# Kernel tuning notes

Measured on AMD Instinct MI355X. Metric: run time of the kernel, lower is better.

Reference implementation:

```python
import jax, jax.numpy as jnp
import numpy as np

N = 100000      # nodes
E = 3_200_000   # edges
F_IN = 256      # input feature dim
R = 16          # rank_bound (GCN output dim)
D = 128         # embedding_dim (trans output)
B = 16384       # batch of node indices
EPS = 1e-5


def setup_inputs() -> dict:
    key = jax.random.key(0)
    ks = jax.random.split(key, 9)
    x = jax.random.normal(ks[0], (N, F_IN), jnp.float32)
    edge_index = jax.random.randint(ks[1], (2, E), 0, N, dtype=jnp.int64)
    trans = jax.random.normal(ks[2], (R, D), jnp.float32) * 0.1
    batch = jax.random.randint(ks[3], (B,), 0, N, dtype=jnp.int64)
    W = jax.random.normal(ks[4], (R, F_IN), jnp.float32) / np.sqrt(F_IN).astype(np.float32)
    b = jnp.zeros((R,), jnp.float32)
    ln_w = jnp.ones((R,), jnp.float32)
    ln_b = jnp.zeros((R,), jnp.float32)
    prelu_a = jnp.full((1,), 0.25, jnp.float32)  # PReLU single shared slope
    return dict(x=x, edge_index=edge_index, trans=trans, batch=batch,
                W=W, b=b, ln_w=ln_w, ln_b=ln_b, prelu_a=prelu_a)


def gcn_conv(x, edge_index, W, b):
    # PyG GCNConv: lin first, then symmetric-normalized aggregation with self-loops.
    h = x @ W.T  # [N, R]
    loop = jnp.arange(N, dtype=edge_index.dtype)
    src = jnp.concatenate([edge_index[0], loop])  # messages flow src -> dst
    dst = jnp.concatenate([edge_index[1], loop])
    deg = jax.ops.segment_sum(jnp.ones_like(dst, h.dtype), dst, num_segments=N)
    dinv = jnp.where(deg > 0, jax.lax.rsqrt(deg), 0.0)
    norm = dinv[src] * dinv[dst]                   # [E+N]
    msg = h[src] * norm[:, None]                   # gather [E+N, R]
    out = jax.ops.segment_sum(msg, dst, num_segments=N)  # scatter-add
    return out + b


def reference(x, edge_index, trans, batch, W, b, ln_w, ln_b, prelu_a):
    h = gcn_conv(x, edge_index, W, b)              # [N, R]
    # PyG LayerNorm (graph mode): normalize over all nodes and channels.
    h = h - h.mean()
    var = (h * h).mean()
    h = h * jax.lax.rsqrt(var + EPS) * ln_w + ln_b
    # PReLU
    h = jnp.where(h >= 0, h, prelu_a * h)
    emb = h @ trans                                # [N, D]
    return emb[batch]                              # index_select(0, batch)
```

## Files before the change

### kernel.cpp

```cpp
#include <hip/hip_runtime.h>

#define EPS 1e-5f
#define BSHIFT 8
#define BSIZE  256
#define NBMAX  512
#define PCHUNK 8192
#define LCAP   12288

__device__ __forceinline__ unsigned short f2bf(float f) {
    unsigned u = __float_as_uint(f);
    u += 0x7FFFu + ((u >> 16) & 1u);
    return (unsigned short)(u >> 16);
}
__device__ __forceinline__ float bf2f(unsigned short s) {
    return __uint_as_float(((unsigned)s) << 16);
}
__device__ __forceinline__ void acc8(float* acc, uint4 v) {
    acc[0] += bf2f((unsigned short)(v.x & 0xFFFFu)); acc[1] += bf2f((unsigned short)(v.x >> 16));
    acc[2] += bf2f((unsigned short)(v.y & 0xFFFFu)); acc[3] += bf2f((unsigned short)(v.y >> 16));
    acc[4] += bf2f((unsigned short)(v.z & 0xFFFFu)); acc[5] += bf2f((unsigned short)(v.z >> 16));
    acc[6] += bf2f((unsigned short)(v.w & 0xFFFFu)); acc[7] += bf2f((unsigned short)(v.w >> 16));
}

__global__ __launch_bounds__(512) void k_zero(unsigned* ghist, int NB) {
    int t = threadIdx.x;
    if (t < NB) ghist[t] = 0u;
}

__global__ __launch_bounds__(512) void k_bhist(const int* __restrict__ ei,
                                               unsigned* __restrict__ ghist,
                                               unsigned* __restrict__ blkhist,
                                               int E, int NB) {
    __shared__ unsigned sh[NBMAX];
    int t = threadIdx.x;
    for (int i = t; i < NB; i += 512) sh[i] = 0u;
    __syncthreads();
    const int4* dst4 = (const int4*)(ei + E);
    int E4 = E >> 2;
    int base4 = blockIdx.x * (PCHUNK / 4);
#pragma unroll
    for (int i = 0; i < PCHUNK / 4 / 512; i++) {
        int idx = base4 + i * 512 + t;
        if (idx < E4) {
            int4 d = dst4[idx];
            atomicAdd(&sh[d.x >> BSHIFT], 1u);
            atomicAdd(&sh[d.y >> BSHIFT], 1u);
            atomicAdd(&sh[d.z >> BSHIFT], 1u);
            atomicAdd(&sh[d.w >> BSHIFT], 1u);
        }
    }
    __syncthreads();
    unsigned* bh = blkhist + (size_t)blockIdx.x * NBMAX;
    for (int i = t; i < NB; i += 512) {
        unsigned c = sh[i];
        bh[i] = c;
        if (c) atomicAdd(&ghist[i], c);
    }
}

__global__ __launch_bounds__(512) void k_bscan(const unsigned* __restrict__ ghist,
                                               unsigned* __restrict__ base,
                                               unsigned* __restrict__ cursor,
                                               unsigned* __restrict__ nstart,
                                               int NB, int N, int E) {
    __shared__ unsigned sh[512];
    int t = threadIdx.x;
    unsigned v = (t < NB) ? ghist[t] : 0u;
    sh[t] = v;
    __syncthreads();
    for (int off = 1; off < 512; off <<= 1) {
        unsigned a = (t >= off) ? sh[t - off] : 0u;
        __syncthreads();
        sh[t] += a;
        __syncthreads();
    }
    if (t < NB) { unsigned ex = sh[t] - v; base[t] = ex; cursor[t] = ex; }
    if (t == 0) { base[NB] = (unsigned)E; nstart[N] = (unsigned)E; }
}

__global__ __launch_bounds__(512) void k_bpart(const int* __restrict__ ei,
                                               const unsigned* __restrict__ blkhist,
                                               unsigned* __restrict__ cursor,
                                               unsigned* __restrict__ sorted, int E, int NB) {
    __shared__ unsigned cnt[NBMAX];
    __shared__ unsigned lbase[NBMAX];
    __shared__ unsigned loff[NBMAX + 1];
    __shared__ unsigned sh[512];
    __shared__ unsigned stage[PCHUNK];
    __shared__ unsigned short bkt[PCHUNK];
    int t = threadIdx.x;
    const unsigned* bh = blkhist + (size_t)blockIdx.x * NBMAX;
    for (int i = t; i < NB; i += 512) cnt[i] = bh[i];
    __syncthreads();
    const int4* src4 = (const int4*)ei;
    const int4* dst4 = (const int4*)(ei + E);
    int E4 = E >> 2;
    int base4 = blockIdx.x * (PCHUNK / 4);
    unsigned v = (t < NB) ? cnt[t] : 0u;
    sh[t] = v;
    if (t < NB) lbase[t] = v ? atomicAdd(&cursor[t], v) : 0u;
    __syncthreads();
    for (int off = 1; off < 512; off <<= 1) {
        unsigned a = (t >= off) ? sh[t - off] : 0u;
        __syncthreads();
        sh[t] += a;
        __syncthreads();
    }
    if (t < NB) { loff[t] = sh[t] - v; cnt[t] = 0u; }
    if (t == NB - 1) loff[NB] = sh[t];
    __syncthreads();
    for (int b = t; b < NB; b += 512) {
        unsigned s = loff[b], e2 = loff[b + 1];
        for (unsigned j = s; j < e2; j++) bkt[j] = (unsigned short)b;
    }
#pragma unroll
    for (int i = 0; i < PCHUNK / 4 / 512; i++) {
        int idx = base4 + i * 512 + t;
        if (idx < E4) {
            int4 s = src4[idx];
            int4 d = dst4[idx];
            int b; unsigned r;
            b = d.x >> BSHIFT; r = atomicAdd(&cnt[b], 1u);
            stage[loff[b] + r] = (unsigned)s.x | ((unsigned)(d.x & (BSIZE - 1)) << 17);
            b = d.y >> BSHIFT; r = atomicAdd(&cnt[b], 1u);
            stage[loff[b] + r] = (unsigned)s.y | ((unsigned)(d.y & (BSIZE - 1)) << 17);
            b = d.z >> BSHIFT; r = atomicAdd(&cnt[b], 1u);
            stage[loff[b] + r] = (unsigned)s.z | ((unsigned)(d.z & (BSIZE - 1)) << 17);
            b = d.w >> BSHIFT; r = atomicAdd(&cnt[b], 1u);
            stage[loff[b] + r] = (unsigned)s.w | ((unsigned)(d.w & (BSIZE - 1)) << 17);
        }
    }
    __syncthreads();
    unsigned total = loff[NB];
    for (unsigned i = t; i < total; i += 512) {
        unsigned b = bkt[i];
        sorted[lbase[b] + (i - loff[b])] = stage[i];
    }
}

__global__ __launch_bounds__(256) void k_bdeg2(const unsigned* __restrict__ base,
                                               const unsigned* __restrict__ sorted,
                                               unsigned* __restrict__ nstart,
                                               float* __restrict__ dinv, int N) {
    __shared__ unsigned deg[BSIZE];
    int b = blockIdx.x, t = threadIdx.x;
    deg[t] = 0u;
    __syncthreads();
    unsigned s0 = base[b], s1 = base[b + 1];
    for (unsigned j = s0 + t; j < s1; j += 256)
        atomicAdd(&deg[sorted[j] >> 17], 1u);
    __syncthreads();
    unsigned d0 = deg[t];
    int lane = t & 63, wid = t >> 6;
    unsigned inc = d0;
    for (int off = 1; off < 64; off <<= 1) {
        unsigned u = __shfl_up(inc, off, 64);
        if (lane >= off) inc += u;
    }
    __shared__ unsigned wsum[4];
    if (lane == 63) wsum[wid] = inc;
    __syncthreads();
    unsigned wbase = 0;
    for (int w = 0; w < wid; w++) wbase += wsum[w];
    unsigned excl = wbase + inc - d0;
    int node = (b << BSHIFT) + t;
    if (node < N) {
        nstart[node] = s0 + excl;
        dinv[node] = rsqrtf((float)(d0 + 1u));
    }
}

__global__ __launch_bounds__(256) void k_gemm(const float* __restrict__ x,
                                              const float* __restrict__ W,
                                              const float* __restrict__ dinv,
                                              unsigned short* __restrict__ hs, int N) {
    __shared__ float ws[16 * 256];
    int t = threadIdx.x;
    for (int i = t; i < 1024; i += 256) ((float4*)ws)[i] = ((const float4*)W)[i];
    __syncthreads();
    int node = blockIdx.x * 256 + t;
    if (node >= N) return;
    const float4* xr = (const float4*)(x + (size_t)node * 256);
    float acc[16];
#pragma unroll
    for (int r = 0; r < 16; r++) acc[r] = 0.f;
#pragma unroll 4
    for (int k = 0; k < 64; k++) {
        float4 a = xr[k];
#pragma unroll
        for (int r = 0; r < 16; r++) {
            float4 w = ((const float4*)ws)[r * 64 + k];
            acc[r] += a.x * w.x + a.y * w.y + a.z * w.z + a.w * w.w;
        }
    }
    float dv = dinv[node];
    unsigned pk[8];
#pragma unroll
    for (int i = 0; i < 8; i++)
        pk[i] = (unsigned)f2bf(acc[2 * i] * dv) | ((unsigned)f2bf(acc[2 * i + 1] * dv) << 16);
    uint4* dst = (uint4*)(hs + (size_t)node * 16);
    dst[0] = make_uint4(pk[0], pk[1], pk[2], pk[3]);
    dst[1] = make_uint4(pk[4], pk[5], pk[6], pk[7]);
}

__global__ __launch_bounds__(256) void k_aggf(const unsigned* __restrict__ base,
                                              const unsigned* __restrict__ nstart,
                                              const unsigned* __restrict__ sorted,
                                              const unsigned short* __restrict__ hs,
                                              const float* __restrict__ dinv,
                                              const float* __restrict__ bias,
                                              float* __restrict__ agg,
                                              float2* __restrict__ part,
                                              unsigned* __restrict__ scratch, int N) {
    __shared__ unsigned buf[LCAP];
    __shared__ unsigned cur0[BSIZE + 1];
    __shared__ unsigned curv[BSIZE];
    __shared__ float ss[4], qq[4];
    int b = blockIdx.x, t = threadIdx.x;
    unsigned s0 = base[b], s1 = base[b + 1];
    unsigned len = s1 - s0;
    int node = (b << BSHIFT) + t;
    unsigned ns = (node < N) ? nstart[node] : s1;
    cur0[t] = ns - s0;
    curv[t] = ns - s0;
    if (t == 0) cur0[BSIZE] = len;
    __syncthreads();
    bool fit = (len <= (unsigned)LCAP);
    if (fit) {
        for (unsigned j = t; j < len; j += 256) {
            unsigned u = sorted[s0 + j];
            unsigned pos = atomicAdd(&curv[u >> 17], 1u);
            buf[pos] = u & 0x1FFFFu;
        }
    } else {
        for (unsigned j = t; j < len; j += 256) {
            unsigned u = sorted[s0 + j];
            unsigned pos = atomicAdd(&curv[u >> 17], 1u);
            scratch[s0 + pos] = u & 0x1FFFFu;
        }
    }
    __syncthreads();
    int g = t >> 4, r = t & 15;
    int sub = r >> 1;
    int half = r & 1;
    float sacc = 0.f, qacc = 0.f;
#pragma unroll 1
    for (int p = 0; p < 16; p++) {
        int dloc = p * 16 + g;
        int d = (b << BSHIFT) + dloc;
        float acc[8];
#pragma unroll
        for (int c = 0; c < 8; c++) acc[c] = 0.f;
        if (d < N) {
            unsigned l0 = cur0[dloc], l1 = cur0[dloc + 1];
            for (unsigned j = l0; j < l1; j += 16) {
                unsigned row0 = j + sub, row1 = j + 8 + sub;
                bool p0 = row0 < l1, p1 = row1 < l1;
                unsigned i0 = 0, i1 = 0;
                if (fit) {
                    if (p0) i0 = buf[row0];
                    if (p1) i1 = buf[row1];
                } else {
                    if (p0) i0 = scratch[s0 + row0];
                    if (p1) i1 = scratch[s0 + row1];
                }
                uint4 v0, v1;
                if (p0) v0 = ((const uint4*)(hs + (size_t)i0 * 16))[half];
                if (p1) v1 = ((const uint4*)(hs + (size_t)i1 * 16))[half];
                if (p0) acc8(acc, v0);
                if (p1) acc8(acc, v1);
            }
        }
#pragma unroll
        for (int off = 2; off <= 8; off <<= 1) {
#pragma unroll
            for (int c = 0; c < 8; c++) acc[c] += __shfl_down(acc[c], off, 64);
        }
        if (d < N && r < 2) {
            float dd = dinv[d];
            uint4 hv = ((const uint4*)(hs + (size_t)d * 16))[half];
            float self[8];
            self[0] = bf2f((unsigned short)(hv.x & 0xFFFFu)); self[1] = bf2f((unsigned short)(hv.x >> 16));
            self[2] = bf2f((unsigned short)(hv.y & 0xFFFFu)); self[3] = bf2f((unsigned short)(hv.y >> 16));
            self[4] = bf2f((unsigned short)(hv.z & 0xFFFFu)); self[5] = bf2f((unsigned short)(hv.z >> 16));
            self[6] = bf2f((unsigned short)(hv.w & 0xFFFFu)); self[7] = bf2f((unsigned short)(hv.w >> 16));
            float o[8];
#pragma unroll
            for (int c = 0; c < 8; c++) o[c] = (acc[c] + self[c]) * dd;
            float* an = agg + (size_t)d * 16 + half * 8;
            *(float4*)(an)     = make_float4(o[0], o[1], o[2], o[3]);
            *(float4*)(an + 4) = make_float4(o[4], o[5], o[6], o[7]);
            const float* bp = bias + half * 8;
            float4 b0 = *(const float4*)bp, b1 = *(const float4*)(bp + 4);
            float a0 = o[0] + b0.x, a1 = o[1] + b0.y, a2 = o[2] + b0.z, a3 = o[3] + b0.w;
            float a4 = o[4] + b1.x, a5 = o[5] + b1.y, a6 = o[6] + b1.z, a7 = o[7] + b1.w;
            sacc += (a0 + a1) + (a2 + a3) + (a4 + a5) + (a6 + a7);
            qacc += a0 * a0 + a1 * a1 + a2 * a2 + a3 * a3 + a4 * a4 + a5 * a5 + a6 * a6 + a7 * a7;
        }
    }
    for (int off = 32; off > 0; off >>= 1) {
        sacc += __shfl_down(sacc, off, 64);
        qacc += __shfl_down(qacc, off, 64);
    }
    int lane = t & 63, wid = t >> 6;
    if (lane == 0) { ss[wid] = sacc; qq[wid] = qacc; }
    __syncthreads();
    if (t == 0)
        part[b] = make_float2(ss[0] + ss[1] + ss[2] + ss[3],
                              qq[0] + qq[1] + qq[2] + qq[3]);
}

__global__ __launch_bounds__(256) void k_statsred(const float2* __restrict__ part,
                                                  float* __restrict__ scal, int M) {
    int t = threadIdx.x;
    float s = 0.f, q = 0.f;
    for (int i = t; i < M; i += 256) {
        float2 v = part[i];
        s += v.x; q += v.y;
    }
    for (int off = 32; off > 0; off >>= 1) {
        s += __shfl_down(s, off, 64);
        q += __shfl_down(q, off, 64);
    }
    __shared__ float ss[4], qq[4];
    int lane = t & 63, wid = t >> 6;
    if (lane == 0) { ss[wid] = s; qq[wid] = q; }
    __syncthreads();
    if (t == 0) {
        scal[0] = ss[0] + ss[1] + ss[2] + ss[3];
        scal[1] = qq[0] + qq[1] + qq[2] + qq[3];
    }
}

__global__ __launch_bounds__(256) void k_final(const float* __restrict__ agg,
                                               const int* __restrict__ batch,
                                               const float* __restrict__ trans,
                                               const float* __restrict__ bias,
                                               const float* __restrict__ ln_w,
                                               const float* __restrict__ ln_b,
                                               const float* __restrict__ prelu_a,
                                               const float* __restrict__ scal,
                                               float* __restrict__ out, int B, float invCnt) {
    __shared__ float tl[16 * 128];
    __shared__ float hh[8 * 16];
    const int tid = threadIdx.x;
    for (int i = tid; i < 2048; i += 256) tl[i] = trans[i];
    float mean = scal[0] * invCnt;
    float var  = scal[1] * invCnt - mean * mean;
    float inv  = rsqrtf(var + EPS);
    int row0 = blockIdx.x * 8;
    if (tid < 128) {
        int lr = tid >> 4, r = tid & 15;
        int row = row0 + lr;
        if (row < B) {
            int node = batch[row];
            float v = agg[(size_t)node * 16 + r] + bias[r];
            v = (v - mean) * inv * ln_w[r] + ln_b[r];
            float a = prelu_a[0];
            v = v >= 0.f ? v : a * v;
            hh[lr * 16 + r] = v;
        }
    }
    __syncthreads();
    int d = tid & 127, hlf = tid >> 7;
    float tv[16];
#pragma unroll
    for (int r = 0; r < 16; r++) tv[r] = tl[r * 128 + d];
#pragma unroll
    for (int rr = 0; rr < 4; rr++) {
        int lr = rr * 2 + hlf;
        int row = row0 + lr;
        if (row < B) {
            const float* hrow = hh + lr * 16;
            float acc = 0.f;
#pragma unroll
            for (int r = 0; r < 16; r++) acc += hrow[r] * tv[r];
            out[(size_t)row * 128 + d] = acc;
        }
    }
}

extern "C" void kernel_launch(void* const* d_in, const int* in_sizes, int n_in,
                              void* d_out, int out_size, void* d_ws, size_t ws_size,
                              hipStream_t stream) {
    const float* x       = (const float*)d_in[0];
    const int*   ei      = (const int*)d_in[1];
    const float* trans   = (const float*)d_in[2];
    const int*   batch   = (const int*)d_in[3];
    const float* W       = (const float*)d_in[4];
    const float* bias    = (const float*)d_in[5];
    const float* ln_w    = (const float*)d_in[6];
    const float* ln_b    = (const float*)d_in[7];
    const float* prelu_a = (const float*)d_in[8];
    float* out = (float*)d_out;

    const int N = in_sizes[0] / 256;
    const int E = in_sizes[1] / 2;
    const int B = in_sizes[3];
    const int NB = (N + BSIZE - 1) >> BSHIFT;
    const int pbp = (E + PCHUNK - 1) / PCHUNK;

    char* p = (char*)d_ws;
    unsigned short* hs = (unsigned short*)p;  p += (size_t)N * 16 * 2;
    float*    agg     = (float*)p;     p += (size_t)N * 16 * 4;
    unsigned* sorted  = (unsigned*)p;  p += (size_t)E * 4;
    unsigned* scratch = (unsigned*)p;  p += (size_t)E * 4;
    unsigned* blkhist = (unsigned*)p;  p += (size_t)pbp * NBMAX * 4;
    float*    dinv    = (float*)p;     p += (size_t)N * 4;
    unsigned* nstart  = (unsigned*)p;  p += (size_t)(N + 1) * 4;
    unsigned* ghist   = (unsigned*)p;  p += NBMAX * 4;
    unsigned* base    = (unsigned*)p;  p += (NBMAX + 1) * 4;
    unsigned* cursor  = (unsigned*)p;  p += NBMAX * 4;
    float*    scal    = (float*)p;     p += 2 * 4;
    p = (char*)(((size_t)p + 7) & ~(size_t)7);
    float2*   part    = (float2*)p;    p += (size_t)NB * 8;

    hipLaunchKernelGGL(k_zero,     dim3(1),               dim3(512), 0, stream, ghist, NB);
    hipLaunchKernelGGL(k_bhist,    dim3(pbp),             dim3(512), 0, stream, ei, ghist, blkhist, E, NB);
    hipLaunchKernelGGL(k_bscan,    dim3(1),               dim3(512), 0, stream, ghist, base, cursor, nstart, NB, N, E);
    hipLaunchKernelGGL(k_bpart,    dim3(pbp),             dim3(512), 0, stream, ei, blkhist, cursor, sorted, E, NB);
    hipLaunchKernelGGL(k_bdeg2,    dim3(NB),              dim3(256), 0, stream, base, sorted, nstart, dinv, N);
    hipLaunchKernelGGL(k_gemm,     dim3((N + 255) / 256), dim3(256), 0, stream, x, W, dinv, hs, N);
    hipLaunchKernelGGL(k_aggf,     dim3(NB),              dim3(256), 0, stream, base, nstart, sorted, hs, dinv, bias, agg, part, scratch, N);
    hipLaunchKernelGGL(k_statsred, dim3(1),               dim3(256), 0, stream, part, scal, NB);
    hipLaunchKernelGGL(k_final,    dim3((B + 7) / 8),     dim3(256), 0, stream, agg, batch, trans, bias,
                       ln_w, ln_b, prelu_a, scal, out, B, 1.0f / (float)(N * 16));
}
```

Before: 302.4 us.

## Rewrite feature projection GEMM with bf16 split-precision MFMA and LDS-staged tiles

```diff
diff --git a/kernel.cpp b/kernel.cpp
--- a/kernel.cpp
+++ b/kernel.cpp
@@ -7,6 +7,9 @@
 #define PCHUNK 8192
 #define LCAP   12288
 
+typedef short bf16x8 __attribute__((ext_vector_type(8)));
+typedef float f32x4  __attribute__((ext_vector_type(4)));
+
 __device__ __forceinline__ unsigned short f2bf(float f) {
     unsigned u = __float_as_uint(f);
     u += 0x7FFFu + ((u >> 16) & 1u);
@@ -20,6 +23,18 @@
     acc[2] += bf2f((unsigned short)(v.y & 0xFFFFu)); acc[3] += bf2f((unsigned short)(v.y >> 16));
     acc[4] += bf2f((unsigned short)(v.z & 0xFFFFu)); acc[5] += bf2f((unsigned short)(v.z >> 16));
     acc[6] += bf2f((unsigned short)(v.w & 0xFFFFu)); acc[7] += bf2f((unsigned short)(v.w >> 16));
+}
+__device__ __forceinline__ void cvt_hilo(const float* f, bf16x8& hi, bf16x8& lo) {
+#pragma unroll
+    for (int j = 0; j < 8; j++) {
+        unsigned short h = f2bf(f[j]);
+        hi[j] = (short)h;
+        lo[j] = (short)f2bf(f[j] - bf2f(h));
+    }
+}
+__device__ __forceinline__ void gload_lds16(const float* g, float* l) {
+    __builtin_amdgcn_global_load_lds((const __attribute__((address_space(1))) void*)g,
+                                     (__attribute__((address_space(3))) void*)l, 16, 0, 0);
 }
 
 __global__ __launch_bounds__(512) void k_zero(unsigned* ghist, int NB) {
@@ -173,34 +188,55 @@
 __global__ __launch_bounds__(256) void k_gemm(const float* __restrict__ x,
                                               const float* __restrict__ W,
                                               const float* __restrict__ dinv,
-                                              unsigned short* __restrict__ hs, int N) {
-    __shared__ float ws[16 * 256];
-    int t = threadIdx.x;
-    for (int i = t; i < 1024; i += 256) ((float4*)ws)[i] = ((const float4*)W)[i];
-    __syncthreads();
-    int node = blockIdx.x * 256 + t;
-    if (node >= N) return;
-    const float4* xr = (const float4*)(x + (size_t)node * 256);
-    float acc[16];
-#pragma unroll
-    for (int r = 0; r < 16; r++) acc[r] = 0.f;
-#pragma unroll 4
-    for (int k = 0; k < 64; k++) {
-        float4 a = xr[k];
-#pragma unroll
-        for (int r = 0; r < 16; r++) {
-            float4 w = ((const float4*)ws)[r * 64 + k];
-            acc[r] += a.x * w.x + a.y * w.y + a.z * w.z + a.w * w.w;
-        }
-    }
-    float dv = dinv[node];
-    unsigned pk[8];
-#pragma unroll
-    for (int i = 0; i < 8; i++)
-        pk[i] = (unsigned)f2bf(acc[2 * i] * dv) | ((unsigned)f2bf(acc[2 * i + 1] * dv) << 16);
-    uint4* dst = (uint4*)(hs + (size_t)node * 16);
-    dst[0] = make_uint4(pk[0], pk[1], pk[2], pk[3]);
-    dst[1] = make_uint4(pk[4], pk[5], pk[6], pk[7]);
+                                              unsigned short* __restrict__ hs,
+                                              int N, int NCH) {
+    __shared__ float xs[64][260];
+    int t = threadIdx.x;
+    int w = t >> 6, lane = t & 63;
+    int lr = lane & 15;
+    int lk = lane >> 4;
+    bf16x8 bh[8], bl[8];
+#pragma unroll
+    for (int kt = 0; kt < 8; kt++) {
+        float wf[8];
+        const float* wp = W + lr * 256 + kt * 32 + lk * 8;
+        *(float4*)&wf[0] = *(const float4*)wp;
+        *(float4*)&wf[4] = *(const float4*)(wp + 4);
+        cvt_hilo(wf, bh[kt], bl[kt]);
+    }
+    for (int ch = blockIdx.x; ch < NCH; ch += gridDim.x) {
+        int cb = ch << 6;
+#pragma unroll
+        for (int j = 0; j < 16; j++) {
+            int row = w * 16 + j;
+            int node = cb + row;
+            if (node < N)
+                gload_lds16(x + (size_t)node * 256 + lane * 4, &xs[row][0]);
+        }
+        __syncthreads();
+        f32x4 acc = {0.f, 0.f, 0.f, 0.f};
+#pragma unroll
+        for (int kt = 0; kt < 8; kt++) {
+            float af[8];
+            const float* ap = &xs[w * 16 + lr][kt * 32 + lk * 8];
+            *(float4*)&af[0] = *(const float4*)ap;
+            *(float4*)&af[4] = *(const float4*)(ap + 4);
+            bf16x8 ah, al;
+            cvt_hilo(af, ah, al);
+            acc = __builtin_amdgcn_mfma_f32_16x16x32_bf16(ah, bh[kt], acc, 0, 0, 0);
+            acc = __builtin_amdgcn_mfma_f32_16x16x32_bf16(al, bh[kt], acc, 0, 0, 0);
+            acc = __builtin_amdgcn_mfma_f32_16x16x32_bf16(ah, bl[kt], acc, 0, 0, 0);
+        }
+#pragma unroll
+        for (int i = 0; i < 4; i++) {
+            int node = cb + w * 16 + lk * 4 + i;
+            if (node < N) {
+                float dv = dinv[node];
+                hs[(size_t)node * 16 + lr] = f2bf(acc[i] * dv);
+            }
+        }
+        __syncthreads();
+    }
 }
 
 __global__ __launch_bounds__(256) void k_aggf(const unsigned* __restrict__ base,
@@ -399,6 +435,7 @@
     const int B = in_sizes[3];
     const int NB = (N + BSIZE - 1) >> BSHIFT;
     const int pbp = (E + PCHUNK - 1) / PCHUNK;
+    const int NCH = (N + 63) / 64;
 
     char* p = (char*)d_ws;
     unsigned short* hs = (unsigned short*)p;  p += (size_t)N * 16 * 2;
@@ -420,7 +457,7 @@
     hipLaunchKernelGGL(k_bscan,    dim3(1),               dim3(512), 0, stream, ghist, base, cursor, nstart, NB, N, E);
     hipLaunchKernelGGL(k_bpart,    dim3(pbp),             dim3(512), 0, stream, ei, blkhist, cursor, sorted, E, NB);
     hipLaunchKernelGGL(k_bdeg2,    dim3(NB),              dim3(256), 0, stream, base, sorted, nstart, dinv, N);
-    hipLaunchKernelGGL(k_gemm,     dim3((N + 255) / 256), dim3(256), 0, stream, x, W, dinv, hs, N);
+    hipLaunchKernelGGL(k_gemm,     dim3(512),             dim3(256), 0, stream, x, W, dinv, hs, N, NCH);
     hipLaunchKernelGGL(k_aggf,     dim3(NB),              dim3(256), 0, stream, base, nstart, sorted, hs, dinv, bias, agg, part, scratch, N);
     hipLaunchKernelGGL(k_statsred, dim3(1),               dim3(256), 0, stream, part, scal, NB);
     hipLaunchKernelGGL(k_final,    dim3((B + 7) / 8),     dim3(256), 0, stream, agg, batch, trans, bias,
```

After: 292.6 us. 3.2% less time.
